# Kernel tuning notes

Hardware: AMD Instinct MI355X
Metric: run time of the kernel (lower is better)

The kernel has to match this reference:

```python
import jax, jax.numpy as jnp
import numpy as np

B, T, D, H, TE = 4, 2048, 1024, 8, 2048
EPS = 1e-5

def _ln(x, w, b):
    m = jnp.mean(x, axis=-1, keepdims=True)
    v = jnp.mean((x - m) ** 2, axis=-1, keepdims=True)
    return (x - m) * jax.lax.rsqrt(v + EPS) * w + b

def setup_inputs() -> dict:
    key = jax.random.key(0)
    ks = jax.random.split(key, 16)
    s = 0.02
    inp = {
        'x': jax.random.normal(ks[0], (B, T, D), jnp.float32),
        'emb': jax.random.normal(ks[1], (B, TE), jnp.float32),
        'src_mask': (jax.random.uniform(ks[2], (B, T, 1)) > 0.2).astype(jnp.float32),
        'num_head': H,
        'ln_w': jnp.ones((D,), jnp.float32),
        'ln_b': jnp.zeros((D,), jnp.float32),
        'Wq': jax.random.normal(ks[3], (D, D), jnp.float32) * s,
        'bq': jnp.zeros((D,), jnp.float32),
        'Wk': jax.random.normal(ks[4], (D, D), jnp.float32) * s,
        'bk': jnp.zeros((D,), jnp.float32),
        'Wv': jax.random.normal(ks[5], (D, D), jnp.float32) * s,
        'bv': jnp.zeros((D,), jnp.float32),
        'W_emb': jax.random.normal(ks[6], (TE, 2 * D), jnp.float32) * s,
        'b_emb': jnp.zeros((2 * D,), jnp.float32),
        'ln2_w': jnp.ones((D,), jnp.float32),
        'ln2_b': jnp.zeros((D,), jnp.float32),
        'W_out': jax.random.normal(ks[7], (D, D), jnp.float32) * s,
        'b_out': jnp.zeros((D,), jnp.float32),
    }
    return inp

def reference(x, emb, src_mask, num_head, ln_w, ln_b, Wq, bq, Wk, bk, Wv, bv,
              W_emb, b_emb, ln2_w, ln2_b, W_out, b_out):
    b, t, d = x.shape
    h = num_head
    dh = d // h
    xn = _ln(x, ln_w, ln_b)
    q = xn @ Wq + bq
    k = xn @ Wk + bk + (1.0 - src_mask) * -1000000.0
    q = jax.nn.softmax(q.reshape(b, t, h, dh), axis=-1)   # feature-map softmax over d_head
    k = jax.nn.softmax(k.reshape(b, t, h, dh), axis=1)    # softmax over time
    v = ((xn @ Wv + bv) * src_mask).reshape(b, t, h, dh)
    att = jnp.einsum('bnhd,bnhl->bhdl', k, v)             # [B,H,dh,dh] KV summary
    y = jnp.einsum('bnhd,bhdl->bnhl', q, att).reshape(b, t, d)
    # StylizationBlock (FiLM), dropout p=0
    emb_out = (jax.nn.silu(emb) @ W_emb + b_emb)[:, None, :]  # [B,1,2D]
    scale, shift = jnp.split(emb_out, 2, axis=2)
    hh = _ln(y, ln2_w, ln2_b) * (1.0 + scale) + shift
    hh = jax.nn.silu(hh) @ W_out + b_out
    return x + hh
```

## Files before the change

kernel.cpp:

```cpp
#include <hip/hip_runtime.h>
#include <hip/hip_bf16.h>

#define B_  4
#define T_  2048
#define D_  1024
#define H_  8
#define DH_ 128
#define TE_ 2048
#define M_  (B_*T_)

using short8 = __attribute__((ext_vector_type(8))) short;
using f32x4  = __attribute__((ext_vector_type(4))) float;

__device__ __forceinline__ ushort f2bf(float f) {
  union { float f; unsigned u; } v; v.f = f;
  unsigned r = (v.u + 0x7fffu + ((v.u >> 16) & 1u)) >> 16;
  return (ushort)r;
}
__device__ __forceinline__ float bf2f(ushort h) {
  union { unsigned u; float f; } v; v.u = ((unsigned)h) << 16;
  return v.f;
}

#define GLOAD_LDS16(g, l) __builtin_amdgcn_global_load_lds( \
    (const __attribute__((address_space(1))) void*)(g), \
    (__attribute__((address_space(3))) void*)(l), 16, 0, 0)

__device__ __forceinline__ void gemm_mainloop(
    const ushort* __restrict__ A, int lda,
    const ushort* __restrict__ Bt, int ldb,
    int K, ushort (*As)[128*32], ushort (*Bs)[128*32], f32x4 acc[4][4])
{
  const int tid  = threadIdx.x;
  const int lane = tid & 63;
  const int wave = tid >> 6;
  const int row  = tid >> 2;
  const int ck   = (tid & 3) * 8;
  const int wm   = (wave & 1) * 64;
  const int wn   = (wave >> 1) * 64;
  const int fr   = lane & 15;
  const int quad = lane >> 4;

  const ushort* ga0 = A  + (size_t)row*lda + ck;
  const ushort* ga1 = A  + (size_t)(row+64)*lda + ck;
  const ushort* gb0 = Bt + (size_t)row*ldb + ck;
  const ushort* gb1 = Bt + (size_t)(row+64)*ldb + ck;
  const int woff = wave*512;

  for (int k0 = 0; k0 < K; k0 += 64) {
    GLOAD_LDS16(ga0 + k0,      As[0] + woff);
    GLOAD_LDS16(ga1 + k0,      As[0] + 2048 + woff);
    GLOAD_LDS16(gb0 + k0,      Bs[0] + woff);
    GLOAD_LDS16(gb1 + k0,      Bs[0] + 2048 + woff);
    GLOAD_LDS16(ga0 + k0 + 32, As[1] + woff);
    GLOAD_LDS16(ga1 + k0 + 32, As[1] + 2048 + woff);
    GLOAD_LDS16(gb0 + k0 + 32, Bs[1] + woff);
    GLOAD_LDS16(gb1 + k0 + 32, Bs[1] + 2048 + woff);
    __syncthreads();
    short8 af[2][4], bw[2][4];
#pragma unroll
    for (int c = 0; c < 2; ++c)
#pragma unroll
      for (int i = 0; i < 4; ++i) {
        af[c][i] = *(const short8*)&As[c][(wm + i*16 + fr)*32 + quad*8];
        bw[c][i] = *(const short8*)&Bs[c][(wn + i*16 + fr)*32 + quad*8];
      }
#pragma unroll
    for (int c = 0; c < 2; ++c)
#pragma unroll
      for (int i = 0; i < 4; ++i)
#pragma unroll
        for (int j = 0; j < 4; ++j)
          acc[i][j] = __builtin_amdgcn_mfma_f32_16x16x32_bf16(af[c][i], bw[c][j], acc[i][j], 0, 0, 0);
    __syncthreads();
  }
}

__global__ __launch_bounds__(256) void gemm_qkv_kernel(
    const ushort* __restrict__ xn, const ushort* __restrict__ Wt,
    const float* __restrict__ bq, const float* __restrict__ bk,
    const float* __restrict__ bv, const float* __restrict__ mask,
    ushort* __restrict__ q, ushort* __restrict__ kT, ushort* __restrict__ vT)
{
  __shared__ __align__(16) ushort As[2][128*32], Bs[2][128*32];
  const int m0 = blockIdx.x * 128;
  const int nt = blockIdx.y;
  f32x4 acc[4][4] = {};
  gemm_mainloop(xn + (size_t)m0*D_, D_, Wt + (size_t)nt*128*D_, D_, D_, As, Bs, acc);

  const int tid = threadIdx.x;
  const int lane = tid & 63, wave = tid >> 6;
  const int wm = (wave & 1)*64, wn = (wave >> 1)*64;
  const int fr = lane & 15, quad = lane >> 4;
  const int grp = nt >> 3;
  const int h = nt & 7;
  const int hbase = h*DH_;

  if (grp == 0) {
    float* redm = (float*)As;
    float* reds = (float*)As + 256;
    const int wi = wn >> 6;
    float bb[4];
#pragma unroll
    for (int j = 0; j < 4; ++j) bb[j] = bq[hbase + wn + j*16 + fr];
#pragma unroll
    for (int i = 0; i < 4; ++i)
#pragma unroll
      for (int r = 0; r < 4; ++r) {
        float m = -1e30f;
#pragma unroll
        for (int j = 0; j < 4; ++j) m = fmaxf(m, acc[i][j][r] + bb[j]);
        m = fmaxf(m, __shfl_xor(m, 1, 64));
        m = fmaxf(m, __shfl_xor(m, 2, 64));
        m = fmaxf(m, __shfl_xor(m, 4, 64));
        m = fmaxf(m, __shfl_xor(m, 8, 64));
        if (fr == 0) redm[(wm + i*16 + quad*4 + r)*2 + wi] = m;
      }
    __syncthreads();
#pragma unroll
    for (int i = 0; i < 4; ++i)
#pragma unroll
      for (int r = 0; r < 4; ++r) {
        int R = wm + i*16 + quad*4 + r;
        float gm = fmaxf(redm[R*2], redm[R*2+1]);
        float s = 0.f;
#pragma unroll
        for (int j = 0; j < 4; ++j) {
          float e = __expf(acc[i][j][r] + bb[j] - gm);
          acc[i][j][r] = e; s += e;
        }
        s += __shfl_xor(s, 1, 64);
        s += __shfl_xor(s, 2, 64);
        s += __shfl_xor(s, 4, 64);
        s += __shfl_xor(s, 8, 64);
        if (fr == 0) reds[R*2 + wi] = s;
      }
    __syncthreads();
#pragma unroll
    for (int i = 0; i < 4; ++i)
#pragma unroll
      for (int r = 0; r < 4; ++r) {
        int R = wm + i*16 + quad*4 + r;
        float inv = 1.0f / (reds[R*2] + reds[R*2+1]);
        size_t m = (size_t)(m0 + R);
#pragma unroll
        for (int j = 0; j < 4; ++j)
          q[m*D_ + hbase + wn + j*16 + fr] = f2bf(acc[i][j][r] * inv);
      }
  } else {
    const float* bias = (grp == 1) ? bk : bv;
    ushort* dstT = (grp == 1) ? kT : vT;
    const int b = m0 >> 11;
    const int t_in_b = m0 & (T_-1);
#pragma unroll
    for (int i = 0; i < 4; ++i)
#pragma unroll
      for (int j = 0; j < 4; ++j) {
        int col = wn + j*16 + fr;
        float bb = bias[hbase + col];
        int t0 = t_in_b + wm + i*16 + quad*4;
        ushort4 pk; ushort* pp = (ushort*)&pk;
#pragma unroll
        for (int r = 0; r < 4; ++r) {
          int m = m0 + wm + i*16 + quad*4 + r;
          float v = acc[i][j][r] + bb;
          if (grp == 1) v += (1.0f - mask[m]) * -1000000.0f;
          else          v *= mask[m];
          pp[r] = f2bf(v);
        }
        *(ushort4*)&dstT[((size_t)(b*H_ + h)*DH_ + col)*T_ + t0] = pk;
      }
  }
}

__global__ __launch_bounds__(256) void ksoftmax_kernel(ushort* __restrict__ kT)
{
  __shared__ float red[8];
  const int row = blockIdx.x;
  const int tid = threadIdx.x;
  ushort* p = &kT[(size_t)row*T_ + tid*8];
  uint4 raw = *(uint4*)p;
  ushort* u = (ushort*)&raw;
  float v[8];
  float mx = -1e30f;
#pragma unroll
  for (int i = 0; i < 8; ++i) { v[i] = bf2f(u[i]); mx = fmaxf(mx, v[i]); }
#pragma unroll
  for (int off = 32; off; off >>= 1) mx = fmaxf(mx, __shfl_xor(mx, off, 64));
  if ((tid & 63) == 0) red[tid >> 6] = mx;
  __syncthreads();
  mx = fmaxf(fmaxf(red[0], red[1]), fmaxf(red[2], red[3]));
  float s = 0.f;
#pragma unroll
  for (int i = 0; i < 8; ++i) { v[i] = __expf(v[i] - mx); s += v[i]; }
#pragma unroll
  for (int off = 32; off; off >>= 1) s += __shfl_xor(s, off, 64);
  if ((tid & 63) == 0) red[4 + (tid >> 6)] = s;
  __syncthreads();
  s = red[4] + red[5] + red[6] + red[7];
  float inv = 1.0f / s;
#pragma unroll
  for (int i = 0; i < 8; ++i) u[i] = f2bf(v[i] * inv);
  *(uint4*)p = raw;
}

__global__ __launch_bounds__(256) void gemm_att_kernel(
    const ushort* __restrict__ kT, const ushort* __restrict__ vT,
    float* __restrict__ P)
{
  __shared__ __align__(16) ushort As[2][128*32], Bs[2][128*32];
  const int bh = blockIdx.x;
  const int s  = blockIdx.y;
  f32x4 acc[4][4] = {};
  gemm_mainloop(kT + (size_t)bh*DH_*T_ + s*256, T_,
                vT + (size_t)bh*DH_*T_ + s*256, T_, 256, As, Bs, acc);
  const int tid = threadIdx.x, lane = tid & 63, wave = tid >> 6;
  const int wm = (wave & 1)*64, wn = (wave >> 1)*64, fr = lane & 15, quad = lane >> 4;
  float* Pb = P + ((size_t)(s*32 + bh))*DH_*DH_;
#pragma unroll
  for (int i = 0; i < 4; ++i)
#pragma unroll
    for (int j = 0; j < 4; ++j) {
      int l = wn + j*16 + fr;
      int d0 = wm + i*16 + quad*4;
      float4 pk = {acc[i][j][0], acc[i][j][1], acc[i][j][2], acc[i][j][3]};
      *(float4*)&Pb[(size_t)l*DH_ + d0] = pk;
    }
}

__global__ __launch_bounds__(256) void att_reduce_kernel(
    const float* __restrict__ P, ushort* __restrict__ attT)
{
  const int e = (blockIdx.x*256 + threadIdx.x) * 4;
  float4 s = {0.f, 0.f, 0.f, 0.f};
#pragma unroll
  for (int k = 0; k < 8; ++k) {
    float4 p = *(const float4*)&P[(size_t)k*32*DH_*DH_ + e];
    s.x += p.x; s.y += p.y; s.z += p.z; s.w += p.w;
  }
  ushort4 o; ushort* op = (ushort*)&o;
  op[0] = f2bf(s.x); op[1] = f2bf(s.y); op[2] = f2bf(s.z); op[3] = f2bf(s.w);
  *(ushort4*)&attT[e] = o;
}

__global__ __launch_bounds__(256) void gemm_y_kernel(
    const ushort* __restrict__ q, const ushort* __restrict__ attT,
    ushort* __restrict__ y)
{
  __shared__ __align__(16) ushort As[2][128*32], Bs[2][128*32];
  const int mt = blockIdx.x;
  const int bh = blockIdx.y;
  const int b = bh >> 3, h = bh & 7;
  const int m0 = b*T_ + mt*128;
  f32x4 acc[4][4] = {};
  gemm_mainloop(q + (size_t)m0*D_ + h*DH_, D_,
                attT + (size_t)bh*DH_*DH_, DH_, DH_, As, Bs, acc);
  const int tid = threadIdx.x, lane = tid & 63, wave = tid >> 6;
  const int wm = (wave & 1)*64, wn = (wave >> 1)*64, fr = lane & 15, quad = lane >> 4;
#pragma unroll
  for (int i = 0; i < 4; ++i)
#pragma unroll
    for (int j = 0; j < 4; ++j) {
      int l = wn + j*16 + fr;
#pragma unroll
      for (int r = 0; r < 4; ++r) {
        int m = m0 + wm + i*16 + quad*4 + r;
        y[(size_t)m*D_ + h*DH_ + l] = f2bf(acc[i][j][r]);
      }
    }
}

__global__ __launch_bounds__(256) void gemm_out_kernel(
    const ushort* __restrict__ act, const ushort* __restrict__ WoutT,
    const float* __restrict__ b_out, const float* __restrict__ x,
    float* __restrict__ out)
{
  __shared__ __align__(16) ushort As[2][128*32], Bs[2][128*32];
  const int m0 = blockIdx.x*128, n0 = blockIdx.y*128;
  f32x4 acc[4][4] = {};
  gemm_mainloop(act + (size_t)m0*D_, D_, WoutT + (size_t)n0*D_, D_, D_, As, Bs, acc);
  const int tid = threadIdx.x, lane = tid & 63, wave = tid >> 6;
  const int wm = (wave & 1)*64, wn = (wave >> 1)*64, fr = lane & 15, quad = lane >> 4;
#pragma unroll
  for (int i = 0; i < 4; ++i)
#pragma unroll
    for (int j = 0; j < 4; ++j) {
      int col = n0 + wn + j*16 + fr;
      float bb = b_out[col];
#pragma unroll
      for (int r = 0; r < 4; ++r) {
        int m = m0 + wm + i*16 + quad*4 + r;
        out[(size_t)m*D_ + col] = acc[i][j][r] + bb + x[(size_t)m*D_ + col];
      }
    }
}

__global__ __launch_bounds__(256) void ln1_kernel(
    const float* __restrict__ x, const float* __restrict__ w,
    const float* __restrict__ bb, ushort* __restrict__ xn)
{
  __shared__ float red[8];
  const int row = blockIdx.x, tid = threadIdx.x;
  const int lane = tid & 63, wave = tid >> 6;
  float4 v = *(const float4*)&x[(size_t)row*D_ + tid*4];
  float s  = v.x + v.y + v.z + v.w;
  float sq = v.x*v.x + v.y*v.y + v.z*v.z + v.w*v.w;
#pragma unroll
  for (int off = 32; off; off >>= 1) { s += __shfl_xor(s, off, 64); sq += __shfl_xor(sq, off, 64); }
  if (lane == 0) { red[wave] = s; red[4+wave] = sq; }
  __syncthreads();
  s  = red[0] + red[1] + red[2] + red[3];
  sq = red[4] + red[5] + red[6] + red[7];
  float mean = s * (1.0f/D_);
  float var  = sq * (1.0f/D_) - mean*mean;
  float rstd = rsqrtf(var + 1e-5f);
  int c = tid*4;
  float vv[4] = {v.x, v.y, v.z, v.w};
  ushort4 o; ushort* op = (ushort*)&o;
#pragma unroll
  for (int i = 0; i < 4; ++i) op[i] = f2bf((vv[i]-mean)*rstd*w[c+i] + bb[c+i]);
  *(ushort4*)&xn[(size_t)row*D_ + c] = o;
}

__global__ __launch_bounds__(256) void ln2_film_kernel(
    const ushort* __restrict__ y, const float* __restrict__ w,
    const float* __restrict__ bb, const float* __restrict__ film,
    const float* __restrict__ b_emb, ushort* __restrict__ act)
{
  __shared__ float red[8];
  const int row = blockIdx.x, tid = threadIdx.x;
  const int lane = tid & 63, wave = tid >> 6;
  const int b = row >> 11;
  ushort4 raw = *(const ushort4*)&y[(size_t)row*D_ + tid*4];
  ushort* u = (ushort*)&raw;
  float v[4];
  float s = 0.f, sq = 0.f;
#pragma unroll
  for (int i = 0; i < 4; ++i) { v[i] = bf2f(u[i]); s += v[i]; sq += v[i]*v[i]; }
#pragma unroll
  for (int off = 32; off; off >>= 1) { s += __shfl_xor(s, off, 64); sq += __shfl_xor(sq, off, 64); }
  if (lane == 0) { red[wave] = s; red[4+wave] = sq; }
  __syncthreads();
  s  = red[0] + red[1] + red[2] + red[3];
  sq = red[4] + red[5] + red[6] + red[7];
  float mean = s * (1.0f/D_);
  float var  = sq * (1.0f/D_) - mean*mean;
  float rstd = rsqrtf(var + 1e-5f);
  int c = tid*4;
  ushort4 o; ushort* op = (ushort*)&o;
#pragma unroll
  for (int i = 0; i < 4; ++i) {
    float yn = (v[i]-mean)*rstd*w[c+i] + bb[c+i];
    float scale = film[b*2048 + c+i]        + b_emb[c+i];
    float shift = film[b*2048 + 1024 + c+i] + b_emb[1024 + c+i];
    float hh = yn*(1.f + scale) + shift;
    op[i] = f2bf(hh / (1.f + __expf(-hh)));
  }
  *(ushort4*)&act[(size_t)row*D_ + c] = o;
}

__global__ __launch_bounds__(256) void film_kernel(
    const float* __restrict__ emb, const float* __restrict__ W_emb,
    float* __restrict__ film)
{
  __shared__ float se[256];
  const int j = blockIdx.x*256 + threadIdx.x;
  const int b = blockIdx.y;
  const int t0 = blockIdx.z*256;
  float e = emb[b*TE_ + t0 + threadIdx.x];
  se[threadIdx.x] = e / (1.f + __expf(-e));
  __syncthreads();
  float acc = 0.f;
  for (int tt = 0; tt < 256; ++tt)
    acc += se[tt] * W_emb[(size_t)(t0+tt)*2048 + j];
  atomicAdd(&film[b*2048 + j], acc);
}

__global__ __launch_bounds__(256) void prep_w_kernel(
    const float* __restrict__ Wq, const float* __restrict__ Wk,
    const float* __restrict__ Wv, const float* __restrict__ Wout,
    ushort* __restrict__ Wqkvt, ushort* __restrict__ WoutT)
{
  __shared__ float tile[32][33];
  const int z = blockIdx.z;
  const float* S = (z == 0) ? Wq : (z == 1) ? Wk : (z == 2) ? Wv : Wout;
  ushort* Dst = (z < 3) ? (Wqkvt + (size_t)z*D_*D_) : WoutT;
  const int n0 = blockIdx.x*32, k0 = blockIdx.y*32;
  const int tx = threadIdx.x & 31, ty = threadIdx.x >> 5;
#pragma unroll
  for (int i = 0; i < 4; ++i)
    tile[ty + i*8][tx] = S[(size_t)(k0 + ty + i*8)*D_ + n0 + tx];
  __syncthreads();
#pragma unroll
  for (int i = 0; i < 4; ++i)
    Dst[(size_t)(n0 + ty + i*8)*D_ + k0 + tx] = f2bf(tile[tx][ty + i*8]);
}

extern "C" void kernel_launch(void* const* d_in, const int* in_sizes, int n_in,
                              void* d_out, int out_size, void* d_ws, size_t ws_size,
                              hipStream_t stream)
{
  const float* x     = (const float*)d_in[0];
  const float* emb   = (const float*)d_in[1];
  const float* mask  = (const float*)d_in[2];
  const float* ln_w  = (const float*)d_in[4];
  const float* ln_b  = (const float*)d_in[5];
  const float* Wq    = (const float*)d_in[6];
  const float* bq    = (const float*)d_in[7];
  const float* Wk    = (const float*)d_in[8];
  const float* bk    = (const float*)d_in[9];
  const float* Wv    = (const float*)d_in[10];
  const float* bv    = (const float*)d_in[11];
  const float* W_emb = (const float*)d_in[12];
  const float* b_emb = (const float*)d_in[13];
  const float* ln2_w = (const float*)d_in[14];
  const float* ln2_b = (const float*)d_in[15];
  const float* Wout  = (const float*)d_in[16];
  const float* b_out = (const float*)d_in[17];
  float* out = (float*)d_out;

  char* ws = (char*)d_ws;
  size_t off = 0;
  auto alloc = [&](size_t bytes) { void* p = ws + off; off += (bytes + 255) & ~size_t(255); return p; };
  ushort* xn    = (ushort*)alloc((size_t)M_*D_*2);
  ushort* q     = (ushort*)alloc((size_t)M_*D_*2);
  ushort* kT    = (ushort*)alloc((size_t)M_*D_*2);
  ushort* vT    = (ushort*)alloc((size_t)M_*D_*2);
  ushort* y     = (ushort*)alloc((size_t)M_*D_*2);
  ushort* Wqkvt = (ushort*)alloc((size_t)3*D_*D_*2);
  ushort* WoutT = (ushort*)alloc((size_t)D_*D_*2);
  ushort* attT  = (ushort*)alloc((size_t)B_*H_*DH_*DH_*2);
  float*  film  = (float*)alloc((size_t)B_*2*D_*4);
  ushort* act   = xn;
  float*  P     = (float*)y;

  hipMemsetAsync(film, 0, (size_t)B_*2*D_*4, stream);
  prep_w_kernel<<<dim3(32, 32, 4), 256, 0, stream>>>(Wq, Wk, Wv, Wout, Wqkvt, WoutT);
  film_kernel<<<dim3(8, 4, 8), 256, 0, stream>>>(emb, W_emb, film);
  ln1_kernel<<<M_, 256, 0, stream>>>(x, ln_w, ln_b, xn);
  gemm_qkv_kernel<<<dim3(64, 24), 256, 0, stream>>>(xn, Wqkvt, bq, bk, bv, mask, q, kT, vT);
  ksoftmax_kernel<<<B_*H_*DH_, 256, 0, stream>>>(kT);
  gemm_att_kernel<<<dim3(32, 8), 256, 0, stream>>>(kT, vT, P);
  att_reduce_kernel<<<512, 256, 0, stream>>>(P, attT);
  gemm_y_kernel<<<dim3(16, 32), 256, 0, stream>>>(q, attT, y);
  ln2_film_kernel<<<M_, 256, 0, stream>>>(y, ln2_w, ln2_b, film, b_emb, act);
  gemm_out_kernel<<<dim3(64, 8), 256, 0, stream>>>(act, WoutT, b_out, x, out);
}
```

Measured before the change: 302.4 us.

## Fuse key time-softmax into QKV GEMM epilogue and pipeline GEMM mainloop

Drops the separate key softmax kernel. The QKV epilogue now stores exp(k) directly and accumulates per-column sums with atomics, and the normalisation by that sum is applied after the KV-summary reduction. Without max subtraction this relies on k values staying small enough that exp does not overflow. The GEMM mainloop also becomes a two-stage software pipeline that prefetches the next 32-wide K slice into the other LDS buffer while the current one is consumed, which changes the barrier pattern.

After: 320.8 us. 1.06x slower.

```diff
diff --git a/kernel.cpp b/kernel.cpp
--- a/kernel.cpp
+++ b/kernel.cpp
@@ -47,32 +47,53 @@
   const ushort* gb1 = Bt + (size_t)(row+64)*ldb + ck;
   const int woff = wave*512;
 
+  GLOAD_LDS16(ga0, As[0] + woff);
+  GLOAD_LDS16(ga1, As[0] + 2048 + woff);
+  GLOAD_LDS16(gb0, Bs[0] + woff);
+  GLOAD_LDS16(gb1, Bs[0] + 2048 + woff);
+
+#pragma unroll 1
   for (int k0 = 0; k0 < K; k0 += 64) {
-    GLOAD_LDS16(ga0 + k0,      As[0] + woff);
-    GLOAD_LDS16(ga1 + k0,      As[0] + 2048 + woff);
-    GLOAD_LDS16(gb0 + k0,      Bs[0] + woff);
-    GLOAD_LDS16(gb1 + k0,      Bs[0] + 2048 + woff);
-    GLOAD_LDS16(ga0 + k0 + 32, As[1] + woff);
-    GLOAD_LDS16(ga1 + k0 + 32, As[1] + 2048 + woff);
-    GLOAD_LDS16(gb0 + k0 + 32, Bs[1] + woff);
-    GLOAD_LDS16(gb1 + k0 + 32, Bs[1] + 2048 + woff);
     __syncthreads();
-    short8 af[2][4], bw[2][4];
-#pragma unroll
-    for (int c = 0; c < 2; ++c)
+    if (k0 + 32 < K) {
+      GLOAD_LDS16(ga0 + k0 + 32, As[1] + woff);
+      GLOAD_LDS16(ga1 + k0 + 32, As[1] + 2048 + woff);
+      GLOAD_LDS16(gb0 + k0 + 32, Bs[1] + woff);
+      GLOAD_LDS16(gb1 + k0 + 32, Bs[1] + 2048 + woff);
+    }
+    {
+      short8 af[4], bw[4];
 #pragma unroll
       for (int i = 0; i < 4; ++i) {
-        af[c][i] = *(const short8*)&As[c][(wm + i*16 + fr)*32 + quad*8];
-        bw[c][i] = *(const short8*)&Bs[c][(wn + i*16 + fr)*32 + quad*8];
-      }
-#pragma unroll
-    for (int c = 0; c < 2; ++c)
+        af[i] = *(const short8*)&As[0][(wm + i*16 + fr)*32 + quad*8];
+        bw[i] = *(const short8*)&Bs[0][(wn + i*16 + fr)*32 + quad*8];
+      }
 #pragma unroll
       for (int i = 0; i < 4; ++i)
 #pragma unroll
         for (int j = 0; j < 4; ++j)
-          acc[i][j] = __builtin_amdgcn_mfma_f32_16x16x32_bf16(af[c][i], bw[c][j], acc[i][j], 0, 0, 0);
+          acc[i][j] = __builtin_amdgcn_mfma_f32_16x16x32_bf16(af[i], bw[j], acc[i][j], 0, 0, 0);
+    }
     __syncthreads();
+    if (k0 + 64 < K) {
+      GLOAD_LDS16(ga0 + k0 + 64, As[0] + woff);
+      GLOAD_LDS16(ga1 + k0 + 64, As[0] + 2048 + woff);
+      GLOAD_LDS16(gb0 + k0 + 64, Bs[0] + woff);
+      GLOAD_LDS16(gb1 + k0 + 64, Bs[0] + 2048 + woff);
+    }
+    {
+      short8 af[4], bw[4];
+#pragma unroll
+      for (int i = 0; i < 4; ++i) {
+        af[i] = *(const short8*)&As[1][(wm + i*16 + fr)*32 + quad*8];
+        bw[i] = *(const short8*)&Bs[1][(wn + i*16 + fr)*32 + quad*8];
+      }
+#pragma unroll
+      for (int i = 0; i < 4; ++i)
+#pragma unroll
+        for (int j = 0; j < 4; ++j)
+          acc[i][j] = __builtin_amdgcn_mfma_f32_16x16x32_bf16(af[i], bw[j], acc[i][j], 0, 0, 0);
+    }
   }
 }
 
@@ -80,7 +101,8 @@
     const ushort* __restrict__ xn, const ushort* __restrict__ Wt,
     const float* __restrict__ bq, const float* __restrict__ bk,
     const float* __restrict__ bv, const float* __restrict__ mask,
-    ushort* __restrict__ q, ushort* __restrict__ kT, ushort* __restrict__ vT)
+    ushort* __restrict__ q, ushort* __restrict__ kT, ushort* __restrict__ vT,
+    float* __restrict__ ksum)
 {
   __shared__ __align__(16) ushort As[2][128*32], Bs[2][128*32];
   const int m0 = blockIdx.x * 128;
@@ -153,55 +175,35 @@
     const int b = m0 >> 11;
     const int t_in_b = m0 & (T_-1);
 #pragma unroll
-    for (int i = 0; i < 4; ++i)
-#pragma unroll
-      for (int j = 0; j < 4; ++j) {
-        int col = wn + j*16 + fr;
-        float bb = bias[hbase + col];
+    for (int j = 0; j < 4; ++j) {
+      int col = wn + j*16 + fr;
+      float bb = bias[hbase + col];
+      float sj = 0.f;
+#pragma unroll
+      for (int i = 0; i < 4; ++i) {
         int t0 = t_in_b + wm + i*16 + quad*4;
         ushort4 pk; ushort* pp = (ushort*)&pk;
 #pragma unroll
         for (int r = 0; r < 4; ++r) {
           int m = m0 + wm + i*16 + quad*4 + r;
           float v = acc[i][j][r] + bb;
-          if (grp == 1) v += (1.0f - mask[m]) * -1000000.0f;
-          else          v *= mask[m];
+          if (grp == 1) {
+            v = __expf(v + (1.0f - mask[m]) * -1000000.0f);
+            sj += v;
+          } else {
+            v *= mask[m];
+          }
           pp[r] = f2bf(v);
         }
         *(ushort4*)&dstT[((size_t)(b*H_ + h)*DH_ + col)*T_ + t0] = pk;
       }
+      if (grp == 1) {
+        sj += __shfl_xor(sj, 16, 64);
+        sj += __shfl_xor(sj, 32, 64);
+        if (quad == 0) atomicAdd(&ksum[(b*H_ + h)*DH_ + col], sj);
+      }
+    }
   }
-}
-
-__global__ __launch_bounds__(256) void ksoftmax_kernel(ushort* __restrict__ kT)
-{
-  __shared__ float red[8];
-  const int row = blockIdx.x;
-  const int tid = threadIdx.x;
-  ushort* p = &kT[(size_t)row*T_ + tid*8];
-  uint4 raw = *(uint4*)p;
-  ushort* u = (ushort*)&raw;
-  float v[8];
-  float mx = -1e30f;
-#pragma unroll
-  for (int i = 0; i < 8; ++i) { v[i] = bf2f(u[i]); mx = fmaxf(mx, v[i]); }
-#pragma unroll
-  for (int off = 32; off; off >>= 1) mx = fmaxf(mx, __shfl_xor(mx, off, 64));
-  if ((tid & 63) == 0) red[tid >> 6] = mx;
-  __syncthreads();
-  mx = fmaxf(fmaxf(red[0], red[1]), fmaxf(red[2], red[3]));
-  float s = 0.f;
-#pragma unroll
-  for (int i = 0; i < 8; ++i) { v[i] = __expf(v[i] - mx); s += v[i]; }
-#pragma unroll
-  for (int off = 32; off; off >>= 1) s += __shfl_xor(s, off, 64);
-  if ((tid & 63) == 0) red[4 + (tid >> 6)] = s;
-  __syncthreads();
-  s = red[4] + red[5] + red[6] + red[7];
-  float inv = 1.0f / s;
-#pragma unroll
-  for (int i = 0; i < 8; ++i) u[i] = f2bf(v[i] * inv);
-  *(uint4*)p = raw;
 }
 
 __global__ __launch_bounds__(256) void gemm_att_kernel(
@@ -229,7 +231,8 @@
 }
 
 __global__ __launch_bounds__(256) void att_reduce_kernel(
-    const float* __restrict__ P, ushort* __restrict__ attT)
+    const float* __restrict__ P, const float* __restrict__ ksum,
+    ushort* __restrict__ attT)
 {
   const int e = (blockIdx.x*256 + threadIdx.x) * 4;
   float4 s = {0.f, 0.f, 0.f, 0.f};
@@ -238,8 +241,12 @@
     float4 p = *(const float4*)&P[(size_t)k*32*DH_*DH_ + e];
     s.x += p.x; s.y += p.y; s.z += p.z; s.w += p.w;
   }
+  const int bh = e >> 14;
+  const int d  = e & 127;
+  const float4 ks = *(const float4*)&ksum[bh*DH_ + d];
   ushort4 o; ushort* op = (ushort*)&o;
-  op[0] = f2bf(s.x); op[1] = f2bf(s.y); op[2] = f2bf(s.z); op[3] = f2bf(s.w);
+  op[0] = f2bf(s.x / ks.x); op[1] = f2bf(s.y / ks.y);
+  op[2] = f2bf(s.z / ks.z); op[3] = f2bf(s.w / ks.w);
   *(ushort4*)&attT[e] = o;
 }
 
@@ -431,17 +438,17 @@
   ushort* WoutT = (ushort*)alloc((size_t)D_*D_*2);
   ushort* attT  = (ushort*)alloc((size_t)B_*H_*DH_*DH_*2);
   float*  film  = (float*)alloc((size_t)B_*2*D_*4);
+  float*  ksum  = (float*)alloc((size_t)B_*H_*DH_*4);
   ushort* act   = xn;
   float*  P     = (float*)y;
 
-  hipMemsetAsync(film, 0, (size_t)B_*2*D_*4, stream);
+  hipMemsetAsync(film, 0, (size_t)(B_*2*D_ + B_*H_*DH_)*4, stream);
   prep_w_kernel<<<dim3(32, 32, 4), 256, 0, stream>>>(Wq, Wk, Wv, Wout, Wqkvt, WoutT);
   film_kernel<<<dim3(8, 4, 8), 256, 0, stream>>>(emb, W_emb, film);
   ln1_kernel<<<M_, 256, 0, stream>>>(x, ln_w, ln_b, xn);
-  gemm_qkv_kernel<<<dim3(64, 24), 256, 0, stream>>>(xn, Wqkvt, bq, bk, bv, mask, q, kT, vT);
-  ksoftmax_kernel<<<B_*H_*DH_, 256, 0, stream>>>(kT);
+  gemm_qkv_kernel<<<dim3(64, 24), 256, 0, stream>>>(xn, Wqkvt, bq, bk, bv, mask, q, kT, vT, ksum);
   gemm_att_kernel<<<dim3(32, 8), 256, 0, stream>>>(kT, vT, P);
-  att_reduce_kernel<<<512, 256, 0, stream>>>(P, attT);
+  att_reduce_kernel<<<512, 256, 0, stream>>>(P, ksum, attT);
   gemm_y_kernel<<<dim3(16, 32), 256, 0, stream>>>(q, attT, y);
   ln2_film_kernel<<<M_, 256, 0, stream>>>(y, ln2_w, ln2_b, film, b_emb, act);
   gemm_out_kernel<<<dim3(64, 8), 256, 0, stream>>>(act, WoutT, b_out, x, out);
```
